# Kernel optimization log

Hardware: AMD Instinct MI355X
Metric: run time of the kernel (lower is better)

The kernel has to match this reference:

```python
import jax, jax.numpy as jnp
import numpy as np

GROUP_SIZE = 128

def setup_inputs() -> dict:
    key = jax.random.key(0)
    k1, k2, k3 = jax.random.split(key, 3)
    B, S, K, N = 4, 128, 4096, 11008
    num_groups = K // GROUP_SIZE
    x = jax.random.normal(k1, (B, S, K), dtype=jnp.float16)
    # packed int4 weights: each byte holds two nibbles (low = even k, high = odd k)
    weight_packed = jax.random.randint(k2, (N, K // 2), 0, 256, dtype=jnp.int32)
    scales = (jax.random.uniform(k3, (N, num_groups), dtype=jnp.float16) * jnp.float16(0.1))
    return {"x": x, "weight_packed": weight_packed, "scales": scales}

def reference(x, weight_packed, scales):
    # x: (B, S, K) fp16; weight_packed: (N, K//2) int in [0,256); scales: (N, K//group_size) fp16
    N, Kp = weight_packed.shape
    K = Kp * 2
    # Unpack nibbles: even k -> low nibble, odd k -> high nibble (interleaved along K)
    low = weight_packed & 0x0F
    high = (weight_packed >> 4) & 0x0F
    w_int = jnp.stack([low, high], axis=-1).reshape(N, K).astype(jnp.float32)  # (N, K)
    # Per-group dequantization: w = scale * (q - 8)
    scale_full = jnp.repeat(scales.astype(jnp.float32), GROUP_SIZE, axis=1)    # (N, K)
    w = scale_full * (w_int - 8.0)
    # fp32 accumulation, fp16 output (matches kernel: float accum, half store)
    y = jnp.einsum('bsk,nk->bsn', x.astype(jnp.float32), w)
    return y.astype(jnp.float16)
```

## Files before the change

### kernel.cpp

```cpp
#include <hip/hip_runtime.h>


typedef __attribute__((ext_vector_type(8)))  short short8;
typedef __attribute__((ext_vector_type(4)))  float f32x4;
typedef __attribute__((ext_vector_type(4)))  int   i32x4;
typedef __attribute__((ext_vector_type(2)))  int   i32x2;
typedef unsigned int   u32;
typedef unsigned short u16;

#define M_DIM 512
#define N_DIM 11008
#define K_DIM 4096
#define BM 128
#define BN 128
#define BK 64
#define KSPLIT 4
#define THREADS 256
#define NTILE_M 4
#define NTILE_N 86
#define NTILES  (NTILE_M * NTILE_N)
#define TILE_EL (BM * BN)

#if defined(__has_builtin)
#  if __has_builtin(__builtin_amdgcn_cvt_pk_bf16_f32)
#    define HAVE_PK_BF16 1
#  endif
#  if __has_builtin(__builtin_amdgcn_global_load_lds)
#    define HAVE_GLLDS 1
#  endif
#endif
#ifndef HAVE_PK_BF16
#  define HAVE_PK_BF16 0
#endif
#ifndef HAVE_GLLDS
#  define HAVE_GLLDS 0
#endif

__device__ __forceinline__ unsigned int fbits(float f) {
    union { float f; unsigned int u; } c; c.f = f; return c.u;
}
__device__ __forceinline__ int pack2bf(float lo, float hi) {
#if HAVE_PK_BF16
    typedef __attribute__((ext_vector_type(2))) __bf16 bf16x2;
    bf16x2 p = __builtin_amdgcn_cvt_pk_bf16_f32(lo, hi);
    int r; __builtin_memcpy(&r, &p, 4);
    return r;
#else
    unsigned int ul = fbits(lo), uh = fbits(hi);
    unsigned int l = (ul + 0x7FFFu + ((ul >> 16) & 1u)) >> 16;
    unsigned int h = (uh + 0x7FFFu + ((uh >> 16) & 1u)) & 0xFFFF0000u;
    return (int)(h | l);
#endif
}

__device__ __forceinline__ void async16(const u16* g, u16* lds) {
#if HAVE_GLLDS
    __builtin_amdgcn_global_load_lds(
        (const __attribute__((address_space(1))) u32*)g,
        (__attribute__((address_space(3))) u32*)lds, 16, 0, 0);
#endif
}

__global__ __launch_bounds__(THREADS)
void cvt_x(const float* __restrict__ x, u16* __restrict__ xw)
{
    int idx = (blockIdx.x * THREADS + threadIdx.x) * 4;
    f32x4 v = *(const f32x4*)(x + idx);
    i32x2 p;
    p[0] = pack2bf(v[0], v[1]);
    p[1] = pack2bf(v[2], v[3]);
    *(i32x2*)(xw + idx) = p;
}

__global__ __launch_bounds__(THREADS, 3)
void dq_gemm_pipe(const u16* __restrict__ xw, const int* __restrict__ wp,
                  const float* __restrict__ scales, float* __restrict__ partials)
{
    __shared__ __align__(16) u16 sA[2][BM * BK];
    __shared__ __align__(16) u16 sB[BN * BK];

    const int t    = threadIdx.x;
    const int lane = t & 63;
    const int wave = t >> 6;
    const int bx   = blockIdx.x;

    int xs = bx & 7, s = bx >> 3;
    const int m_idx = s & 3;
    int q = (s >> 2) * 8 + xs;
    const int ksp = q & 3;
    const int nb  = q >> 2;
    const int m0 = m_idx * BM;
    const int n0 = nb * BN;
    const int k0 = ksp * (K_DIM / KSPLIT);
    const int KITERS = (K_DIM / KSPLIT) / BK;

    const int wm = (wave & 1) * 64;
    const int wn = (wave >> 1) * 64;
    const int lm   = lane & 15;
    const int quad = lane >> 4;

    int rowi[4], kcgi[4];
    #pragma unroll
    for (int i = 0; i < 4; ++i) {
        int ci = i * 256 + t;
        rowi[i] = ci >> 3;
        kcgi[i] = (ci & 7) ^ (rowi[i] & 7);
    }

    f32x4 acc[4][4] = {};
    i32x4 pv[4];
    float sc[4];

    auto load_b = [&](int kb) {
        #pragma unroll
        for (int i = 0; i < 4; ++i) {
            pv[i] = *(const i32x4*)(wp + (size_t)(n0 + rowi[i]) * (K_DIM / 2)
                                    + (kb >> 1) + kcgi[i] * 4);
            sc[i] = scales[(size_t)(n0 + rowi[i]) * 32 + (kb >> 7)];
        }
    };
    auto load_a_async = [&](int kb, int buf) {
#if HAVE_GLLDS
        #pragma unroll
        for (int i = 0; i < 4; ++i) {
            u16* lb = sA[buf] + (size_t)(i * 256 + wave * 64) * 8;
            async16(xw + (size_t)(m0 + rowi[i]) * K_DIM + kb + kcgi[i] * 8, lb);
        }
#else
        #pragma unroll
        for (int i = 0; i < 4; ++i) {
            int ci = i * 256 + t;
            *(i32x4*)(sA[buf] + (size_t)ci * 8) =
                *(const i32x4*)(xw + (size_t)(m0 + rowi[i]) * K_DIM + kb + kcgi[i] * 8);
        }
#endif
    };
    auto dequant_b = [&]() {
        #pragma unroll
        for (int i = 0; i < 4; ++i) {
            int ci = i * 256 + t;
            float sf = sc[i], ns8 = sf * -8.0f;
            i32x4 res;
            #pragma unroll
            for (int e = 0; e < 4; ++e) {
                int b = pv[i][e];
                res[e] = pack2bf((float)(b & 15) * sf + ns8,
                                 (float)((b >> 4) & 15) * sf + ns8);
            }
            *(i32x4*)(sB + (size_t)ci * 8) = res;
        }
    };

    load_b(k0);
    load_a_async(k0, 0);
    dequant_b();
    __syncthreads();

    for (int kk = 0; kk < KITERS; ++kk) {
        const bool has_next = (kk + 1 < KITERS);
        const int kb_next = k0 + (kk + 1) * BK;
        if (has_next) {
            load_b(kb_next);
            load_a_async(kb_next, (kk + 1) & 1);
        }

        const u16* sAc = sA[kk & 1];
        #pragma unroll
        for (int ks = 0; ks < BK; ks += 32) {
            const int kc = (ks >> 3) + quad;
            short8 a[4], b[4];
            #pragma unroll
            for (int i = 0; i < 4; ++i) {
                int row = wm + i * 16 + lm;
                a[i] = *(const short8*)&sAc[(row * 8 + (kc ^ (row & 7))) * 8];
            }
            #pragma unroll
            for (int j = 0; j < 4; ++j) {
                int row = wn + j * 16 + lm;
                b[j] = *(const short8*)&sB[(row * 8 + (kc ^ (row & 7))) * 8];
            }
            #pragma unroll
            for (int i = 0; i < 4; ++i)
                #pragma unroll
                for (int j = 0; j < 4; ++j)
                    acc[i][j] = __builtin_amdgcn_mfma_f32_16x16x32_bf16(
                        a[i], b[j], acc[i][j], 0, 0, 0);
        }

        __syncthreads();
        if (has_next) {
            dequant_b();
            __syncthreads();
        }
    }

    float* my = partials + ((size_t)(m_idx * NTILE_N + nb) * KSPLIT + ksp) * TILE_EL;
    #pragma unroll
    for (int i = 0; i < 4; ++i)
        #pragma unroll
        for (int j = 0; j < 4; ++j)
            *(f32x4*)(my + (i * 4 + j) * 1024 + t * 4) = acc[i][j];
}

template<bool PRECVT>
__global__ __launch_bounds__(THREADS, 2)
void dq_gemm_basic(const u16* __restrict__ xw, const float* __restrict__ xf,
                   const int* __restrict__ wp, const float* __restrict__ scales,
                   float* __restrict__ out)
{
    __shared__ __align__(16) u16 sA[BM * BK];
    __shared__ __align__(16) u16 sB[BN * BK];

    const int t    = threadIdx.x;
    const int lane = t & 63;
    const int wave = t >> 6;
    const int m_idx = blockIdx.x & 3, nb = blockIdx.x >> 2;
    const int m0 = m_idx * BM, n0 = nb * BN;

    const int wm = (wave & 1) * 64, wn = (wave >> 1) * 64;
    const int lm = lane & 15, quad = lane >> 4;

    f32x4 acc[4][4] = {};

    for (int kb = 0; kb < K_DIM; kb += BK) {
        const int g = kb >> 7;
        i32x4 pv[4];
        float sc[4];
        #pragma unroll
        for (int i = 0; i < 4; ++i) {
            int ci = i * 256 + t, row = ci >> 3;
            int kcg = (ci & 7) ^ (row & 7);
            pv[i] = *(const i32x4*)(wp + (size_t)(n0 + row) * (K_DIM / 2) + (kb >> 1) + kcg * 4);
            sc[i] = scales[(size_t)(n0 + row) * 32 + g];
        }
        if constexpr (PRECVT) {
            #pragma unroll
            for (int i = 0; i < 4; ++i) {
                int ci = i * 256 + t, row = ci >> 3;
                int kcg = (ci & 7) ^ (row & 7);
                *(i32x4*)(sA + (size_t)ci * 8) =
                    *(const i32x4*)(xw + (size_t)(m0 + row) * K_DIM + kb + kcg * 8);
            }
        } else {
            #pragma unroll
            for (int i = 0; i < 8; ++i) {
                int c = i * 256 + t;
                int row = c >> 4, col4 = (c & 15) * 4;
                int kc = col4 >> 3, half = (col4 >> 2) & 1;
                f32x4 v = *(const f32x4*)(xf + (size_t)(m0 + row) * K_DIM + kb + col4);
                i32x2 p;
                p[0] = pack2bf(v[0], v[1]);
                p[1] = pack2bf(v[2], v[3]);
                *(i32x2*)(sA + (size_t)(row * 8 + (kc ^ (row & 7))) * 8 + half * 4) = p;
            }
        }
        #pragma unroll
        for (int i = 0; i < 4; ++i) {
            int ci = i * 256 + t;
            float sf = sc[i], ns8 = sf * -8.0f;
            i32x4 res;
            #pragma unroll
            for (int e = 0; e < 4; ++e) {
                int b = pv[i][e];
                res[e] = pack2bf((float)(b & 15) * sf + ns8,
                                 (float)((b >> 4) & 15) * sf + ns8);
            }
            *(i32x4*)(sB + (size_t)ci * 8) = res;
        }
        __syncthreads();
        #pragma unroll
        for (int ks = 0; ks < BK; ks += 32) {
            const int kc = (ks >> 3) + quad;
            short8 a[4], b[4];
            #pragma unroll
            for (int i = 0; i < 4; ++i) {
                int row = wm + i * 16 + lm;
                a[i] = *(const short8*)&sA[(row * 8 + (kc ^ (row & 7))) * 8];
            }
            #pragma unroll
            for (int j = 0; j < 4; ++j) {
                int row = wn + j * 16 + lm;
                b[j] = *(const short8*)&sB[(row * 8 + (kc ^ (row & 7))) * 8];
            }
            #pragma unroll
            for (int i = 0; i < 4; ++i)
                #pragma unroll
                for (int j = 0; j < 4; ++j)
                    acc[i][j] = __builtin_amdgcn_mfma_f32_16x16x32_bf16(
                        a[i], b[j], acc[i][j], 0, 0, 0);
        }
        __syncthreads();
    }

    #pragma unroll
    for (int i = 0; i < 4; ++i) {
        int mg = m0 + wm + i * 16 + quad * 4;
        #pragma unroll
        for (int j = 0; j < 4; ++j) {
            int ng = n0 + wn + j * 16 + lm;
            #pragma unroll
            for (int r = 0; r < 4; ++r)
                out[(size_t)(mg + r) * N_DIM + ng] = acc[i][j][r];
        }
    }
}

__global__ __launch_bounds__(THREADS)
void reduce_k(const float* __restrict__ partials, float* __restrict__ out)
{
    __shared__ float sT[64][132];

    const int b    = blockIdx.x;
    const int tile = b >> 1;
    const int h    = b & 1;
    const int m_idx = tile / NTILE_N;
    const int nb    = tile % NTILE_N;
    const int m0 = m_idx * BM + h * 64;
    const int n0 = nb * BN;
    const int u  = threadIdx.x;

    const float* base = partials + (size_t)tile * KSPLIT * TILE_EL;

    #pragma unroll
    for (int it = 0; it < 8; ++it) {
        int idx = it * 256 + u;
        int c   = idx >> 7;
        int tl  = idx & 127;
        int t   = (tl & 63) | (h << 6) | ((tl >> 6) << 7);
        int off = c * 1024 + t * 4;
        f32x4 s = *(const f32x4*)(base + off);
        s += *(const f32x4*)(base + TILE_EL + off);
        s += *(const f32x4*)(base + 2 * TILE_EL + off);
        s += *(const f32x4*)(base + 3 * TILE_EL + off);
        int i = c >> 2, j = c & 3;
        int lane = t & 63, wave = t >> 6;
        int mrow = i * 16 + (lane >> 4) * 4;
        int ncol = (wave >> 1) * 64 + j * 16 + (lane & 15);
        sT[mrow + 0][ncol] = s[0];
        sT[mrow + 1][ncol] = s[1];
        sT[mrow + 2][ncol] = s[2];
        sT[mrow + 3][ncol] = s[3];
    }
    __syncthreads();

    #pragma unroll
    for (int it = 0; it < 8; ++it) {
        int idx = it * 256 + u;
        int row = idx >> 5;
        int c4  = (idx & 31) * 4;
        f32x4 v = *(const f32x4*)&sT[row][c4];
        *(f32x4*)(out + (size_t)(m0 + row) * N_DIM + n0 + c4) = v;
    }
}

extern "C" void kernel_launch(void* const* d_in, const int* in_sizes, int n_in,
                              void* d_out, int out_size, void* d_ws, size_t ws_size,
                              hipStream_t stream) {
    (void)in_sizes; (void)n_in; (void)out_size;
    const float* x      = (const float*)d_in[0];
    const int*   wpck   = (const int*)d_in[1];
    const float* scales = (const float*)d_in[2];
    float*       out    = (float*)d_out;

    const size_t XW_BYTES   = (size_t)M_DIM * K_DIM * 2;
    const size_t PART_OFF   = XW_BYTES;
    const size_t PART_BYTES = (size_t)NTILES * KSPLIT * TILE_EL * 4;

    if (ws_size >= PART_OFF + PART_BYTES) {
        u16*   xw   = (u16*)d_ws;
        float* part = (float*)((char*)d_ws + PART_OFF);
        cvt_x<<<(M_DIM * K_DIM) / (THREADS * 4), THREADS, 0, stream>>>(x, xw);
        dq_gemm_pipe<<<NTILES * KSPLIT, THREADS, 0, stream>>>(xw, wpck, scales, part);
        reduce_k<<<NTILES * 2, THREADS, 0, stream>>>(part, out);
    } else if (ws_size >= XW_BYTES) {
        u16* xw = (u16*)d_ws;
        cvt_x<<<(M_DIM * K_DIM) / (THREADS * 4), THREADS, 0, stream>>>(x, xw);
        dq_gemm_basic<true><<<NTILES, THREADS, 0, stream>>>(
            xw, x, wpck, scales, out);
    } else {
        dq_gemm_basic<false><<<NTILES, THREADS, 0, stream>>>(
            nullptr, x, wpck, scales, out);
    }
}
```

Baseline: 227.4 us.

## Double-buffer dequantized B tile and prefetch packed weights two steps ahead

Restructures the split-K GEMM main loop so the dequantized weight tile in LDS is double-buffered and packed weights are prefetched two iterations ahead into register slots. Dequantization of the next tile now runs before the MFMAs on the current tile, so one of the two barriers per iteration goes away. It also replaces the bf16 pack with a cheaper round-half-up byte-permute version, drops the high-nibble mask, and lowers the occupancy hint from 3 to 2 blocks to accommodate the extra LDS and registers. The rounding change can differ slightly from round-to-nearest-even, and the lower occupancy may reduce latency hiding.

```diff
diff --git a/kernel.cpp b/kernel.cpp
--- a/kernel.cpp
+++ b/kernel.cpp
@@ -22,16 +22,10 @@
 #define TILE_EL (BM * BN)
 
 #if defined(__has_builtin)
-#  if __has_builtin(__builtin_amdgcn_cvt_pk_bf16_f32)
-#    define HAVE_PK_BF16 1
-#  endif
 #  if __has_builtin(__builtin_amdgcn_global_load_lds)
 #    define HAVE_GLLDS 1
 #  endif
 #endif
-#ifndef HAVE_PK_BF16
-#  define HAVE_PK_BF16 0
-#endif
 #ifndef HAVE_GLLDS
 #  define HAVE_GLLDS 0
 #endif
@@ -40,17 +34,15 @@
     union { float f; unsigned int u; } c; c.f = f; return c.u;
 }
 __device__ __forceinline__ int pack2bf(float lo, float hi) {
-#if HAVE_PK_BF16
-    typedef __attribute__((ext_vector_type(2))) __bf16 bf16x2;
-    bf16x2 p = __builtin_amdgcn_cvt_pk_bf16_f32(lo, hi);
-    int r; __builtin_memcpy(&r, &p, 4);
-    return r;
-#else
     unsigned int ul = fbits(lo), uh = fbits(hi);
     unsigned int l = (ul + 0x7FFFu + ((ul >> 16) & 1u)) >> 16;
     unsigned int h = (uh + 0x7FFFu + ((uh >> 16) & 1u)) & 0xFFFF0000u;
     return (int)(h | l);
-#endif
+}
+__device__ __forceinline__ int pack2bf_fast(float lo, float hi) {
+    unsigned int u0 = fbits(lo) + 0x8000u;
+    unsigned int u1 = fbits(hi) + 0x8000u;
+    return (int)__builtin_amdgcn_perm(u1, u0, 0x07060302u);
 }
 
 __device__ __forceinline__ void async16(const u16* g, u16* lds) {
@@ -72,12 +64,12 @@
     *(i32x2*)(xw + idx) = p;
 }
 
-__global__ __launch_bounds__(THREADS, 3)
+__global__ __launch_bounds__(THREADS, 2)
 void dq_gemm_pipe(const u16* __restrict__ xw, const int* __restrict__ wp,
                   const float* __restrict__ scales, float* __restrict__ partials)
 {
     __shared__ __align__(16) u16 sA[2][BM * BK];
-    __shared__ __align__(16) u16 sB[BN * BK];
+    __shared__ __align__(16) u16 sB[2][BN * BK];
 
     const int t    = threadIdx.x;
     const int lane = t & 63;
@@ -92,6 +84,7 @@
     const int m0 = m_idx * BM;
     const int n0 = nb * BN;
     const int k0 = ksp * (K_DIM / KSPLIT);
+    const int g0 = k0 >> 7;
     const int KITERS = (K_DIM / KSPLIT) / BK;
 
     const int wm = (wave & 1) * 64;
@@ -100,71 +93,63 @@
     const int quad = lane >> 4;
 
     int rowi[4], kcgi[4];
+    const int*   pb[4];
+    const float* ps[4];
+    const u16*   pa[4];
     #pragma unroll
     for (int i = 0; i < 4; ++i) {
         int ci = i * 256 + t;
         rowi[i] = ci >> 3;
         kcgi[i] = (ci & 7) ^ (rowi[i] & 7);
+        pb[i] = wp + (size_t)(n0 + rowi[i]) * (K_DIM / 2) + (k0 >> 1) + kcgi[i] * 4;
+        ps[i] = scales + (size_t)(n0 + rowi[i]) * 32;
+        pa[i] = xw + (size_t)(m0 + rowi[i]) * K_DIM + k0 + kcgi[i] * 8;
     }
 
     f32x4 acc[4][4] = {};
-    i32x4 pv[4];
-    float sc[4];
-
-    auto load_b = [&](int kb) {
-        #pragma unroll
-        for (int i = 0; i < 4; ++i) {
-            pv[i] = *(const i32x4*)(wp + (size_t)(n0 + rowi[i]) * (K_DIM / 2)
-                                    + (kb >> 1) + kcgi[i] * 4);
-            sc[i] = scales[(size_t)(n0 + rowi[i]) * 32 + (kb >> 7)];
-        }
-    };
-    auto load_a_async = [&](int kb, int buf) {
+    i32x4 pv[2][4];
+    float sc[2][4];
+
+    auto issue_b = [&](int slot, int kk) {
+        #pragma unroll
+        for (int i = 0; i < 4; ++i) {
+            pv[slot][i] = *(const i32x4*)(pb[i] + kk * (BK / 2));
+            sc[slot][i] = ps[i][g0 + (kk >> 1)];
+        }
+    };
+    auto issue_a = [&](int kk, int buf) {
 #if HAVE_GLLDS
         #pragma unroll
         for (int i = 0; i < 4; ++i) {
             u16* lb = sA[buf] + (size_t)(i * 256 + wave * 64) * 8;
-            async16(xw + (size_t)(m0 + rowi[i]) * K_DIM + kb + kcgi[i] * 8, lb);
+            async16(pa[i] + kk * BK, lb);
         }
 #else
         #pragma unroll
         for (int i = 0; i < 4; ++i) {
             int ci = i * 256 + t;
-            *(i32x4*)(sA[buf] + (size_t)ci * 8) =
-                *(const i32x4*)(xw + (size_t)(m0 + rowi[i]) * K_DIM + kb + kcgi[i] * 8);
+            *(i32x4*)(sA[buf] + (size_t)ci * 8) = *(const i32x4*)(pa[i] + kk * BK);
         }
 #endif
     };
-    auto dequant_b = [&]() {
+    auto dequant_to = [&](int slot, int buf) {
         #pragma unroll
         for (int i = 0; i < 4; ++i) {
             int ci = i * 256 + t;
-            float sf = sc[i], ns8 = sf * -8.0f;
+            float sf = sc[slot][i], ns8 = sf * -8.0f;
             i32x4 res;
             #pragma unroll
             for (int e = 0; e < 4; ++e) {
-                int b = pv[i][e];
-                res[e] = pack2bf((float)(b & 15) * sf + ns8,
-                                 (float)((b >> 4) & 15) * sf + ns8);
-            }
-            *(i32x4*)(sB + (size_t)ci * 8) = res;
-        }
-    };
-
-    load_b(k0);
-    load_a_async(k0, 0);
-    dequant_b();
-    __syncthreads();
-
-    for (int kk = 0; kk < KITERS; ++kk) {
-        const bool has_next = (kk + 1 < KITERS);
-        const int kb_next = k0 + (kk + 1) * BK;
-        if (has_next) {
-            load_b(kb_next);
-            load_a_async(kb_next, (kk + 1) & 1);
-        }
-
-        const u16* sAc = sA[kk & 1];
+                int b = pv[slot][i][e];
+                res[e] = pack2bf_fast((float)(b & 15) * sf + ns8,
+                                      (float)(b >> 4) * sf + ns8);
+            }
+            *(i32x4*)(sB[buf] + (size_t)ci * 8) = res;
+        }
+    };
+    auto mfma_tile = [&](int buf) {
+        const u16* sAc = sA[buf];
+        const u16* sBc = sB[buf];
         #pragma unroll
         for (int ks = 0; ks < BK; ks += 32) {
             const int kc = (ks >> 3) + quad;
@@ -177,7 +162,7 @@
             #pragma unroll
             for (int j = 0; j < 4; ++j) {
                 int row = wn + j * 16 + lm;
-                b[j] = *(const short8*)&sB[(row * 8 + (kc ^ (row & 7))) * 8];
+                b[j] = *(const short8*)&sBc[(row * 8 + (kc ^ (row & 7))) * 8];
             }
             #pragma unroll
             for (int i = 0; i < 4; ++i)
@@ -186,12 +171,24 @@
                     acc[i][j] = __builtin_amdgcn_mfma_f32_16x16x32_bf16(
                         a[i], b[j], acc[i][j], 0, 0, 0);
         }
-
+    };
+
+    issue_b(0, 0);
+    issue_a(0, 0);
+    dequant_to(0, 0);
+    issue_b(1, 1);
+    __syncthreads();
+
+    auto step = [&](int kk, int p) {
+        if (kk + 1 < KITERS) issue_a(kk + 1, p ^ 1);
+        if (kk + 2 < KITERS) issue_b(p, kk + 2);
+        if (kk + 1 < KITERS) dequant_to(p ^ 1, p ^ 1);
+        mfma_tile(p);
         __syncthreads();
-        if (has_next) {
-            dequant_b();
-            __syncthreads();
-        }
+    };
+    for (int kk = 0; kk < KITERS; kk += 2) {
+        step(kk, 0);
+        step(kk + 1, 1);
     }
 
     float* my = partials + ((size_t)(m_idx * NTILE_N + nb) * KSPLIT + ksp) * TILE_EL;
@@ -262,8 +259,8 @@
             #pragma unroll
             for (int e = 0; e < 4; ++e) {
                 int b = pv[i][e];
-                res[e] = pack2bf((float)(b & 15) * sf + ns8,
-                                 (float)((b >> 4) & 15) * sf + ns8);
+                res[e] = pack2bf_fast((float)(b & 15) * sf + ns8,
+                                      (float)(b >> 4) * sf + ns8);
             }
             *(i32x4*)(sB + (size_t)ci * 8) = res;
         }
```

After: 226.6 us. No clear change (-0.4%).
